# Optimization experiments

Measured on AMD Instinct MI355X. Metric: run time of the kernel, lower is better.

## Reference

```python
import jax, jax.numpy as jnp
import numpy as np

D_MODEL = 1024


def setup_inputs() -> dict:
    key = jax.random.key(0)
    k1, k2, k3 = jax.random.split(key, 3)
    x = jax.random.normal(k1, (4, 2048, D_MODEL), dtype=jnp.float32)
    w_qkv = jax.random.normal(k2, (D_MODEL, 3 * D_MODEL), dtype=jnp.float32) * (D_MODEL ** -0.5)
    b_qkv = jnp.zeros((3 * D_MODEL,), dtype=jnp.float32)
    w_out = jax.random.normal(k3, (D_MODEL, D_MODEL), dtype=jnp.float32) * (D_MODEL ** -0.5)
    b_out = jnp.zeros((D_MODEL,), dtype=jnp.float32)
    return {"x": x, "w_qkv": w_qkv, "b_qkv": b_qkv, "w_out": w_out, "b_out": b_out}


def reference(x, w_qkv, b_qkv, w_out, b_out):
    # x: [B, S, D]
    d_model = x.shape[-1]
    scale = jnp.asarray(d_model, x.dtype) ** 0.5
    qkv = x @ w_qkv + b_qkv                      # [B, S, 3D]
    q, k, v = jnp.split(qkv, 3, axis=-1)          # each [B, S, D]
    scores = jnp.einsum('bsd,btd->bst', q, k) / scale  # [B, S, S]
    attn = jax.nn.softmax(scores, axis=-1)
    out = jnp.einsum('bst,btd->bsd', attn, v)     # [B, S, D]
    return out @ w_out + b_out
```

## Files before the change

### kernel.cpp

```cpp
#include <hip/hip_runtime.h>
#include <hip/hip_bf16.h>
#include <cstdint>

typedef __attribute__((ext_vector_type(8))) short bf16x8;
typedef __attribute__((ext_vector_type(4))) float f32x4;
using bf16 = __hip_bfloat16;

static __device__ __forceinline__ float tofloat(float x) { return x; }
static __device__ __forceinline__ float tofloat(bf16 x) { return __bfloat162float(x); }
static __device__ __forceinline__ void storeval(float* p, float v) { *p = v; }
static __device__ __forceinline__ void storeval(bf16* p, float v) { *p = __float2bfloat16(v); }

#define MFMA_BF16 __builtin_amdgcn_mfma_f32_16x16x32_bf16

template <int N>
static __device__ __forceinline__ void vm_wait() {
    if constexpr (N == 0) asm volatile("s_waitcnt vmcnt(0)" ::: "memory");
    else if constexpr (N == 6) asm volatile("s_waitcnt vmcnt(6)" ::: "memory");
    else if constexpr (N == 8) asm volatile("s_waitcnt vmcnt(8)" ::: "memory");
}
static __device__ __forceinline__ void lgkm0() {
    asm volatile("s_waitcnt lgkmcnt(0)" ::: "memory");
    __builtin_amdgcn_sched_barrier(0);
}
static __device__ __forceinline__ void phase_bar() {
    __builtin_amdgcn_sched_barrier(0);
    __builtin_amdgcn_s_barrier();
    __builtin_amdgcn_sched_barrier(0);
}
static __device__ __forceinline__ void gl_lds(const bf16* src, char* dst) {
    __builtin_amdgcn_global_load_lds((const __attribute__((address_space(1))) unsigned int*)src,
                                     (__attribute__((address_space(3))) unsigned int*)dst, 16, 0, 0);
}

__global__ __launch_bounds__(256) void convert_f32_bf16(const float* __restrict__ in,
                                                        bf16* __restrict__ out, long n) {
    long i = ((long)blockIdx.x * blockDim.x + threadIdx.x) * 8;
    if (i >= n) return;
    float4 a = *(const float4*)(in + i);
    float4 b = *(const float4*)(in + i + 4);
    bf16 t[8];
    t[0] = __float2bfloat16(a.x); t[1] = __float2bfloat16(a.y);
    t[2] = __float2bfloat16(a.z); t[3] = __float2bfloat16(a.w);
    t[4] = __float2bfloat16(b.x); t[5] = __float2bfloat16(b.y);
    t[6] = __float2bfloat16(b.z); t[7] = __float2bfloat16(b.w);
    *(uint4*)(out + i) = *(const uint4*)t;
}

template <typename SrcT>
__global__ __launch_bounds__(256) void transpose_to_bf16(const SrcT* __restrict__ src, long srcStride,
                                                         long srcBatch, bf16* __restrict__ dst,
                                                         long dstStride, long dstBatch) {
    __shared__ float tile[32][33];
    const SrcT* s = src + (long)blockIdx.z * srcBatch;
    bf16* d = dst + (long)blockIdx.z * dstBatch;
    long r0 = (long)blockIdx.y * 32, c0 = (long)blockIdx.x * 32;
    for (int i = threadIdx.y; i < 32; i += 8)
        tile[i][threadIdx.x] = tofloat(s[(r0 + i) * srcStride + c0 + threadIdx.x]);
    __syncthreads();
    for (int i = threadIdx.y; i < 32; i += 8)
        d[(c0 + i) * dstStride + r0 + threadIdx.x] = __float2bfloat16(tile[threadIdx.x][i]);
}

template <typename OutT, bool BIAS, int BM>
__global__ __launch_bounds__(512, 2) void gemm8p(
    const bf16* __restrict__ Ag, long lda, long batchA,
    const bf16* __restrict__ Bg, long ldb, long batchB,
    OutT* __restrict__ Cg, long ldc, long batchC,
    const float* __restrict__ bias, int K, float alpha) {
    constexpr int MR = BM / 32;
    constexpr int LA = BM / 128;
    constexpr int PA = BM * 64;
    constexpr int PB = 16384;
    constexpr int WV = 4 + 2 * LA;
    extern __shared__ __align__(16) char smem[];

    const int tid = threadIdx.x;
    const int wave = tid >> 6, lane = tid & 63, l16 = lane & 15, lhi = lane >> 4;
    const int wm = wave >> 2, wn = wave & 3;

    const long mtile = (long)blockIdx.y * BM;
    const long ntile = (long)blockIdx.x * 256;
    const bf16* A = Ag + (long)blockIdx.z * batchA;
    const bf16* B = Bg + (long)blockIdx.z * batchB;
    OutT* C = Cg + (long)blockIdx.z * batchC;

    const int rp0 = tid >> 3;
    const int g8 = ((tid & 7) ^ ((tid >> 4) & 7)) * 8;
    const bf16* pA = A + (mtile + rp0) * lda + g8;
    const bf16* pB = B + (ntile + rp0) * ldb + g8;
    const int wb = wave * 1024;

    auto stageB = [&](int par, int t) {
        const bf16* s0 = pB + (long)t * 64;
        char* d0 = smem + 4 * PA + par * PB + wb;
        gl_lds(s0, d0);
        gl_lds(s0 + 64 * ldb, d0 + 8192);
        const bf16* s1 = s0 + 128 * ldb;
        char* d1 = smem + 4 * PA + 2 * PB + par * PB + wb;
        gl_lds(s1, d1);
        gl_lds(s1 + 64 * ldb, d1 + 8192);
    };
    auto stageA = [&](int par, int t) {
        const bf16* s0 = pA + (long)t * 64;
        char* d0 = smem + par * PA + wb;
        gl_lds(s0, d0);
        if constexpr (LA == 2) gl_lds(s0 + 64 * lda, d0 + 8192);
        const bf16* s1 = s0 + (long)(BM / 2) * lda;
        char* d1 = smem + 2 * PA + par * PA + wb;
        gl_lds(s1, d1);
        if constexpr (LA == 2) gl_lds(s1 + 64 * lda, d1 + 8192);
    };

    const int swz = (l16 >> 1) & 7;
    const int cb0 = (lhi ^ swz) * 16;
    const int cb1 = ((4 + lhi) ^ swz) * 16;
    const char* aBase = smem + wm * 2 * PA + l16 * 128;
    const char* bBase = smem + 4 * PA + (wn >> 1) * 2 * PB + ((wn & 1) * 64 + l16) * 128;

    bf16x8 aq[MR], bq[8];
    f32x4 acc[MR][4];
#pragma unroll
    for (int m = 0; m < MR; ++m)
#pragma unroll
        for (int n = 0; n < 4; ++n) acc[m][n] = f32x4{0.f, 0.f, 0.f, 0.f};

#define LDA_(par, h)                                                           \
    do {                                                                       \
        const char* p_ = aBase + (par) * PA + (h) * (PA / 2);                  \
        _Pragma("unroll")                                                      \
        for (int m_ = 0; m_ < MR / 2; ++m_) {                                  \
            aq[2 * m_]     = *(const bf16x8*)(p_ + m_ * 2048 + cb0);           \
            aq[2 * m_ + 1] = *(const bf16x8*)(p_ + m_ * 2048 + cb1);           \
        }                                                                      \
    } while (0)

#define LDB_(par, nlo)                                                         \
    do {                                                                       \
        const char* p_ = bBase + (par) * PB + (nlo) * 2048;                    \
        bq[(nlo) * 2 + 0] = *(const bf16x8*)(p_ + cb0);                        \
        bq[(nlo) * 2 + 1] = *(const bf16x8*)(p_ + cb1);                        \
        bq[(nlo) * 2 + 2] = *(const bf16x8*)(p_ + 2048 + cb0);                 \
        bq[(nlo) * 2 + 3] = *(const bf16x8*)(p_ + 2048 + cb1);                 \
    } while (0)

#define QUAD_(h, nlo)                                                          \
    do {                                                                       \
        __builtin_amdgcn_s_setprio(1);                                         \
        _Pragma("unroll")                                                      \
        for (int m_ = 0; m_ < MR / 2; ++m_) {                                  \
            acc[(h) * (MR / 2) + m_][(nlo) + 0] =                              \
                MFMA_BF16(aq[2 * m_], bq[(nlo) * 2 + 0], acc[(h) * (MR / 2) + m_][(nlo) + 0], 0, 0, 0); \
            acc[(h) * (MR / 2) + m_][(nlo) + 0] =                              \
                MFMA_BF16(aq[2 * m_ + 1], bq[(nlo) * 2 + 1], acc[(h) * (MR / 2) + m_][(nlo) + 0], 0, 0, 0); \
            acc[(h) * (MR / 2) + m_][(nlo) + 1] =                              \
                MFMA_BF16(aq[2 * m_], bq[(nlo) * 2 + 2], acc[(h) * (MR / 2) + m_][(nlo) + 1], 0, 0, 0); \
            acc[(h) * (MR / 2) + m_][(nlo) + 1] =                              \
                MFMA_BF16(aq[2 * m_ + 1], bq[(nlo) * 2 + 3], acc[(h) * (MR / 2) + m_][(nlo) + 1], 0, 0, 0); \
        }                                                                      \
        __builtin_amdgcn_s_setprio(0);                                         \
    } while (0)

#define KTILE(par, tstage, MODE)                                               \
    do {                                                                       \
        LDA_(par, 0); LDB_(par, 0);                                    \
        phase_bar(); lgkm0();                                                  \
        QUAD_(0, 0);                                                           \
        phase_bar();                                                           \
        LDB_(par, 2);                                                  \
        phase_bar(); lgkm0();                                                  \
        QUAD_(0, 2);                                                           \
        phase_bar();                                                           \
        LDA_(par, 1);                                                  \
        if (MODE == 0) stageB(par, tstage);                                    \
        phase_bar(); lgkm0();                                                  \
        QUAD_(1, 2);                                                           \
        phase_bar();                                                           \
        if (MODE == 0) stageA(par, tstage);                            \
        QUAD_(1, 0);                                                           \
        if (MODE == 0) vm_wait<WV>();                                          \
        if (MODE == 1) vm_wait<0>();                                           \
        phase_bar();                                                           \
    } while (0)

    const int NT = K / 64;

    stageB(0, 0); stageA(0, 0);
    stageB(1, 1); stageA(1, 1);
    vm_wait<WV>();
    phase_bar();

    for (int t = 0; t < NT - 2; ++t) KTILE(t & 1, t + 2, 0);
    KTILE(0, 0, 1);
    KTILE(1, 0, 2);

#pragma unroll
    for (int n = 0; n < 4; ++n) {
        long col = ntile + wn * 64 + n * 16 + l16;
        float bv = BIAS ? bias[col] : 0.0f;
#pragma unroll
        for (int am = 0; am < MR; ++am) {
            const int h_ = am / (MR / 2), mm = am % (MR / 2);
            long row = mtile + wm * (BM / 2) + h_ * (BM / 4) + mm * 16 + lhi * 4;
#pragma unroll
            for (int r2 = 0; r2 < 4; ++r2)
                storeval(&C[(row + r2) * ldc + col], acc[am][n][r2] * alpha + bv);
        }
    }
#undef KTILE
#undef QUAD_
#undef LDB_
#undef LDA_
}

__global__ __launch_bounds__(256) void softmax_rows(float* __restrict__ S, int ncols) {
    __shared__ float red[8];
    const long row = blockIdx.x;
    float* srow = S + row * ncols;
    const int tid = threadIdx.x;
    float v[8];
    float4 x0 = ((const float4*)srow)[tid * 2];
    float4 x1 = ((const float4*)srow)[tid * 2 + 1];
    v[0] = x0.x; v[1] = x0.y; v[2] = x0.z; v[3] = x0.w;
    v[4] = x1.x; v[5] = x1.y; v[6] = x1.z; v[7] = x1.w;
    float m = -3.4e38f;
#pragma unroll
    for (int j = 0; j < 8; ++j) m = fmaxf(m, v[j]);
#pragma unroll
    for (int off = 32; off; off >>= 1) m = fmaxf(m, __shfl_xor(m, off));
    if ((tid & 63) == 0) red[tid >> 6] = m;
    __syncthreads();
    m = fmaxf(fmaxf(red[0], red[1]), fmaxf(red[2], red[3]));
    float s = 0.0f;
#pragma unroll
    for (int j = 0; j < 8; ++j) {
        v[j] = __expf(v[j] - m);
        s += v[j];
    }
#pragma unroll
    for (int off = 32; off; off >>= 1) s += __shfl_xor(s, off);
    if ((tid & 63) == 0) red[4 + (tid >> 6)] = s;
    __syncthreads();
    s = red[4] + red[5] + red[6] + red[7];
    float inv = 1.0f / s;
    bf16 o[8];
#pragma unroll
    for (int j = 0; j < 8; ++j) o[j] = __float2bfloat16(v[j] * inv);
    *(uint4*)((bf16*)srow + tid * 8) = *(const uint4*)o;
}

extern "C" void kernel_launch(void* const* d_in, const int* in_sizes, int n_in, void* d_out,
                              int out_size, void* d_ws, size_t ws_size, hipStream_t stream) {
    (void)in_sizes; (void)n_in; (void)out_size;
    const float* x = (const float*)d_in[0];
    const float* w_qkv = (const float*)d_in[1];
    const float* b_qkv = (const float*)d_in[2];
    const float* w_out = (const float*)d_in[3];
    const float* b_out = (const float*)d_in[4];
    float* out = (float*)d_out;

    const int B = 4, S = 2048, D = 1024;

    {
        (void)hipFuncSetAttribute((const void*)&gemm8p<bf16, true, 256>,
                                  hipFuncAttributeMaxDynamicSharedMemorySize, 131072);
        (void)hipFuncSetAttribute((const void*)&gemm8p<float, false, 256>,
                                  hipFuncAttributeMaxDynamicSharedMemorySize, 131072);
        (void)hipFuncSetAttribute((const void*)&gemm8p<bf16, false, 128>,
                                  hipFuncAttributeMaxDynamicSharedMemorySize, 98304);
        (void)hipFuncSetAttribute((const void*)&gemm8p<float, true, 128>,
                                  hipFuncAttributeMaxDynamicSharedMemorySize, 98304);
    }

    char* ws = (char*)d_ws;
    size_t off = 0;
    auto alloc = [&](size_t bytes) {
        char* p = ws + off;
        off += (bytes + 255) & ~(size_t)255;
        return p;
    };
    bf16* xb = (bf16*)alloc((size_t)B * S * D * 2);
    bf16* qkv = (bf16*)alloc((size_t)B * S * 3 * D * 2);
    bf16* wqkvT = (bf16*)alloc((size_t)3 * D * D * 2);
    bf16* woutT = (bf16*)alloc((size_t)D * D * 2);
    bf16* vt = (bf16*)alloc((size_t)B * D * S * 2);
    bf16* ao = (bf16*)alloc((size_t)B * S * D * 2);
    size_t sc_bytes_full = (size_t)B * S * S * 4;
    int NB = (ws_size >= off + sc_bytes_full) ? B : 1;
    float* sc = (float*)alloc((size_t)NB * S * S * 4);

    long nx = (long)B * S * D;
    convert_f32_bf16<<<(int)(nx / 8 / 256), 256, 0, stream>>>(x, xb, nx);

    dim3 tb(32, 8);
    transpose_to_bf16<float><<<dim3(3 * D / 32, D / 32, 1), tb, 0, stream>>>(
        w_qkv, 3 * D, 0, wqkvT, D, 0);
    transpose_to_bf16<float><<<dim3(D / 32, D / 32, 1), tb, 0, stream>>>(
        w_out, D, 0, woutT, D, 0);

    gemm8p<bf16, true, 256><<<dim3(3 * D / 256, B * S / 256, 1), 512, 131072, stream>>>(
        xb, D, 0, wqkvT, D, 0, qkv, 3 * D, 0, b_qkv, D, 1.0f);

    transpose_to_bf16<bf16><<<dim3(D / 32, S / 32, B), tb, 0, stream>>>(
        qkv + 2 * D, 3 * D, (long)S * 3 * D, vt, S, (long)D * S);

    for (int b0 = 0; b0 < B; b0 += NB) {
        const bf16* Qb = qkv + (size_t)b0 * S * 3 * D;
        const bf16* Kb = Qb + D;
        gemm8p<float, false, 256><<<dim3(S / 256, S / 256, NB), 512, 131072, stream>>>(
            Qb, 3 * D, (long)S * 3 * D, Kb, 3 * D, (long)S * 3 * D,
            sc, S, (long)S * S, nullptr, D, 0.03125f);
        softmax_rows<<<NB * S, 256, 0, stream>>>(sc, S);
        gemm8p<bf16, false, 128><<<dim3(D / 256, S / 128, NB), 512, 98304, stream>>>(
            (const bf16*)sc, 2 * S, (long)S * 2 * S,
            vt + (size_t)b0 * D * S, S, (long)D * S,
            ao + (size_t)b0 * S * D, D, (long)S * D, nullptr, S, 1.0f);
    }

    gemm8p<float, true, 128><<<dim3(D / 256, B * S / 128, 1), 512, 98304, stream>>>(
        ao, D, 0, woutT, D, 0, out, D, 0, b_out, D, 1.0f);
}
```

Baseline: 222.1 us.

## Store attention scores in bf16, remap GEMM tiles across XCDs, relax barriers

The QK^T GEMM now writes bf16 scores, and softmax reads and writes bf16 in place, so the score matrix takes half the memory traffic. The old per-batch loop and its workspace fallback are removed, so all batches go through one launch per stage. GEMMs now use a flat 1D grid with an XCD-aware remap of block index to tile, aiming for better L2 locality across chiplets. Full scheduling barriers are replaced with plain s_barrier plus partial sched fences, giving the compiler more freedom to interleave work. Rounding scores to bf16 before softmax costs some accuracy, and the workspace must now hold all batches' scores at once.

```diff
diff --git a/kernel.cpp b/kernel.cpp
--- a/kernel.cpp
+++ b/kernel.cpp
@@ -23,11 +23,8 @@
     asm volatile("s_waitcnt lgkmcnt(0)" ::: "memory");
     __builtin_amdgcn_sched_barrier(0);
 }
-static __device__ __forceinline__ void phase_bar() {
-    __builtin_amdgcn_sched_barrier(0);
-    __builtin_amdgcn_s_barrier();
-    __builtin_amdgcn_sched_barrier(0);
-}
+static __device__ __forceinline__ void bar() { __builtin_amdgcn_s_barrier(); }
+static __device__ __forceinline__ void vmem_fence() { __builtin_amdgcn_sched_barrier(0x38F); }
 static __device__ __forceinline__ void gl_lds(const bf16* src, char* dst) {
     __builtin_amdgcn_global_load_lds((const __attribute__((address_space(1))) unsigned int*)src,
                                      (__attribute__((address_space(3))) unsigned int*)dst, 16, 0, 0);
@@ -67,7 +64,7 @@
     const bf16* __restrict__ Ag, long lda, long batchA,
     const bf16* __restrict__ Bg, long ldb, long batchB,
     OutT* __restrict__ Cg, long ldc, long batchC,
-    const float* __restrict__ bias, int K, float alpha) {
+    const float* __restrict__ bias, int K, float alpha, int nx, int ny) {
     constexpr int MR = BM / 32;
     constexpr int LA = BM / 128;
     constexpr int PA = BM * 64;
@@ -79,11 +76,16 @@
     const int wave = tid >> 6, lane = tid & 63, l16 = lane & 15, lhi = lane >> 4;
     const int wm = wave >> 2, wn = wave & 3;
 
-    const long mtile = (long)blockIdx.y * BM;
-    const long ntile = (long)blockIdx.x * 256;
-    const bf16* A = Ag + (long)blockIdx.z * batchA;
-    const bf16* B = Bg + (long)blockIdx.z * batchB;
-    OutT* C = Cg + (long)blockIdx.z * batchC;
+    const int nwg = gridDim.x;
+    const int l = (blockIdx.x & 7) * (nwg >> 3) + (blockIdx.x >> 3);
+    const int pt = nx * ny;
+    const int z = l / pt, rr = l % pt;
+    const long mtile = (long)(rr / nx) * BM;
+    const long ntile = (long)(rr % nx) * 256;
+
+    const bf16* A = Ag + (long)z * batchA;
+    const bf16* B = Bg + (long)z * batchB;
+    OutT* C = Cg + (long)z * batchC;
 
     const int rp0 = tid >> 3;
     const int g8 = ((tid & 7) ^ ((tid >> 4) & 7)) * 8;
@@ -163,24 +165,28 @@
 
 #define KTILE(par, tstage, MODE)                                               \
     do {                                                                       \
-        LDA_(par, 0); LDB_(par, 0);                                    \
-        phase_bar(); lgkm0();                                                  \
+                                                                       \
+        LDA_(par, 0); LDB_(par, 0);                                            \
+        bar(); lgkm0();                                                        \
         QUAD_(0, 0);                                                           \
-        phase_bar();                                                           \
-        LDB_(par, 2);                                                  \
-        phase_bar(); lgkm0();                                                  \
+        bar();                                                                 \
+                                                                       \
+        LDB_(par, 2);                                                          \
+        bar(); lgkm0();                                                        \
         QUAD_(0, 2);                                                           \
-        phase_bar();                                                           \
-        LDA_(par, 1);                                                  \
+        bar(); vmem_fence();                                                   \
+            \
+        LDA_(par, 1);                                                          \
         if (MODE == 0) stageB(par, tstage);                                    \
-        phase_bar(); lgkm0();                                                  \
+        bar(); lgkm0();                                                        \
         QUAD_(1, 2);                                                           \
-        phase_bar();                                                           \
-        if (MODE == 0) stageA(par, tstage);                            \
+        bar(); vmem_fence();                                                   \
+                             \
+        if (MODE == 0) stageA(par, tstage);                                    \
         QUAD_(1, 0);                                                           \
         if (MODE == 0) vm_wait<WV>();                                          \
         if (MODE == 1) vm_wait<0>();                                           \
-        phase_bar();                                                           \
+        bar();                                                                 \
     } while (0)
 
     const int NT = K / 64;
@@ -188,7 +194,7 @@
     stageB(0, 0); stageA(0, 0);
     stageB(1, 1); stageA(1, 1);
     vm_wait<WV>();
-    phase_bar();
+    bar();
 
     for (int t = 0; t < NT - 2; ++t) KTILE(t & 1, t + 2, 0);
     KTILE(0, 0, 1);
@@ -213,16 +219,16 @@
 #undef LDA_
 }
 
-__global__ __launch_bounds__(256) void softmax_rows(float* __restrict__ S, int ncols) {
+__global__ __launch_bounds__(256) void softmax_rows_bf16(bf16* __restrict__ S, int ncols) {
     __shared__ float red[8];
     const long row = blockIdx.x;
-    float* srow = S + row * ncols;
+    bf16* srow = S + row * ncols;
     const int tid = threadIdx.x;
+    uint4 raw = *(const uint4*)(srow + tid * 8);
+    const bf16* rb = (const bf16*)&raw;
     float v[8];
-    float4 x0 = ((const float4*)srow)[tid * 2];
-    float4 x1 = ((const float4*)srow)[tid * 2 + 1];
-    v[0] = x0.x; v[1] = x0.y; v[2] = x0.z; v[3] = x0.w;
-    v[4] = x1.x; v[5] = x1.y; v[6] = x1.z; v[7] = x1.w;
+#pragma unroll
+    for (int j = 0; j < 8; ++j) v[j] = __bfloat162float(rb[j]);
     float m = -3.4e38f;
 #pragma unroll
     for (int j = 0; j < 8; ++j) m = fmaxf(m, v[j]);
@@ -246,12 +252,12 @@
     bf16 o[8];
 #pragma unroll
     for (int j = 0; j < 8; ++j) o[j] = __float2bfloat16(v[j] * inv);
-    *(uint4*)((bf16*)srow + tid * 8) = *(const uint4*)o;
+    *(uint4*)(srow + tid * 8) = *(const uint4*)o;
 }
 
 extern "C" void kernel_launch(void* const* d_in, const int* in_sizes, int n_in, void* d_out,
                               int out_size, void* d_ws, size_t ws_size, hipStream_t stream) {
-    (void)in_sizes; (void)n_in; (void)out_size;
+    (void)in_sizes; (void)n_in; (void)out_size; (void)ws_size;
     const float* x = (const float*)d_in[0];
     const float* w_qkv = (const float*)d_in[1];
     const float* b_qkv = (const float*)d_in[2];
@@ -264,7 +270,7 @@
     {
         (void)hipFuncSetAttribute((const void*)&gemm8p<bf16, true, 256>,
                                   hipFuncAttributeMaxDynamicSharedMemorySize, 131072);
-        (void)hipFuncSetAttribute((const void*)&gemm8p<float, false, 256>,
+        (void)hipFuncSetAttribute((const void*)&gemm8p<bf16, false, 256>,
                                   hipFuncAttributeMaxDynamicSharedMemorySize, 131072);
         (void)hipFuncSetAttribute((const void*)&gemm8p<bf16, false, 128>,
                                   hipFuncAttributeMaxDynamicSharedMemorySize, 98304);
@@ -285,12 +291,10 @@
     bf16* woutT = (bf16*)alloc((size_t)D * D * 2);
     bf16* vt = (bf16*)alloc((size_t)B * D * S * 2);
     bf16* ao = (bf16*)alloc((size_t)B * S * D * 2);
-    size_t sc_bytes_full = (size_t)B * S * S * 4;
-    int NB = (ws_size >= off + sc_bytes_full) ? B : 1;
-    float* sc = (float*)alloc((size_t)NB * S * S * 4);
-
-    long nx = (long)B * S * D;
-    convert_f32_bf16<<<(int)(nx / 8 / 256), 256, 0, stream>>>(x, xb, nx);
+    bf16* sc = (bf16*)alloc((size_t)B * S * S * 2);
+
+    long nx_ = (long)B * S * D;
+    convert_f32_bf16<<<(int)(nx_ / 8 / 256), 256, 0, stream>>>(x, xb, nx_);
 
     dim3 tb(32, 8);
     transpose_to_bf16<float><<<dim3(3 * D / 32, D / 32, 1), tb, 0, stream>>>(
@@ -298,25 +302,22 @@
     transpose_to_bf16<float><<<dim3(D / 32, D / 32, 1), tb, 0, stream>>>(
         w_out, D, 0, woutT, D, 0);
 
-    gemm8p<bf16, true, 256><<<dim3(3 * D / 256, B * S / 256, 1), 512, 131072, stream>>>(
-        xb, D, 0, wqkvT, D, 0, qkv, 3 * D, 0, b_qkv, D, 1.0f);
+    gemm8p<bf16, true, 256><<<384, 512, 131072, stream>>>(
+        xb, D, 0, wqkvT, D, 0, qkv, 3 * D, 0, b_qkv, D, 1.0f, 3 * D / 256, B * S / 256);
 
     transpose_to_bf16<bf16><<<dim3(D / 32, S / 32, B), tb, 0, stream>>>(
         qkv + 2 * D, 3 * D, (long)S * 3 * D, vt, S, (long)D * S);
 
-    for (int b0 = 0; b0 < B; b0 += NB) {
-        const bf16* Qb = qkv + (size_t)b0 * S * 3 * D;
-        const bf16* Kb = Qb + D;
-        gemm8p<float, false, 256><<<dim3(S / 256, S / 256, NB), 512, 131072, stream>>>(
-            Qb, 3 * D, (long)S * 3 * D, Kb, 3 * D, (long)S * 3 * D,
-            sc, S, (long)S * S, nullptr, D, 0.03125f);
-        softmax_rows<<<NB * S, 256, 0, stream>>>(sc, S);
-        gemm8p<bf16, false, 128><<<dim3(D / 256, S / 128, NB), 512, 98304, stream>>>(
-            (const bf16*)sc, 2 * S, (long)S * 2 * S,
-            vt + (size_t)b0 * D * S, S, (long)D * S,
-            ao + (size_t)b0 * S * D, D, (long)S * D, nullptr, S, 1.0f);
-    }
-
-    gemm8p<float, true, 128><<<dim3(D / 256, B * S / 128, 1), 512, 98304, stream>>>(
-        ao, D, 0, woutT, D, 0, out, D, 0, b_out, D, 1.0f);
-}
+    gemm8p<bf16, false, 256><<<256, 512, 131072, stream>>>(
+        qkv, 3 * D, (long)S * 3 * D, qkv + D, 3 * D, (long)S * 3 * D,
+        sc, S, (long)S * S, nullptr, D, 0.03125f, S / 256, S / 256);
+
+    softmax_rows_bf16<<<B * S, 256, 0, stream>>>(sc, S);
+
+    gemm8p<bf16, false, 128><<<256, 512, 98304, stream>>>(
+        sc, S, (long)S * S, vt, S, (long)D * S,
+        ao, D, (long)S * D, nullptr, S, 1.0f, D / 256, S / 128);
+
+    gemm8p<float, true, 128><<<256, 512, 98304, stream>>>(
+        ao, D, 0, woutT, D, 0, out, D, 0, b_out, D, 1.0f, D / 256, B * S / 128);
+}
```

Result: faster. 211.2 us (-4.9%).
